# Performance work log

Measured on AMD Instinct MI355X. Metric: run time of the kernel, lower is better.

## Reference

```python
import jax, jax.numpy as jnp
import numpy as np

C = 256
CQK = C // 8  # query/key channels = int(in_dim // 8)

def _conv1x1(x, W, b):
    # x: [B,C,H,W], W: [O,C], b: [O] -> [B,O,H,W]
    return jnp.einsum('bchw,oc->bohw', x, W) + b[None, :, None, None]

def setup_inputs() -> dict:
    key = jax.random.key(0)
    ks = jax.random.split(key, 9)
    B, H, W = 4, 64, 64
    s = lambda fan_in: 1.0 / np.sqrt(fan_in)
    x = jax.random.normal(ks[0], (B, C, H, W), dtype=jnp.float32)
    Wq = jax.random.uniform(ks[1], (CQK, C), jnp.float32, -s(C), s(C))
    bq = jax.random.uniform(ks[2], (CQK,), jnp.float32, -s(C), s(C))
    Wk = jax.random.uniform(ks[3], (CQK, C), jnp.float32, -s(C), s(C))
    bk = jax.random.uniform(ks[4], (CQK,), jnp.float32, -s(C), s(C))
    Wv = jax.random.uniform(ks[5], (C, C), jnp.float32, -s(C), s(C))
    bv = jax.random.uniform(ks[6], (C,), jnp.float32, -s(C), s(C))
    Wo = jax.random.uniform(ks[7], (C, 2 * C), jnp.float32, -s(2 * C), s(2 * C))
    bo = jax.random.uniform(ks[8], (C,), jnp.float32, -s(2 * C), s(2 * C))
    return {"x": x, "Wq": Wq, "bq": bq, "Wk": Wk, "bk": bk,
            "Wv": Wv, "bv": bv, "Wo": Wo, "bo": bo}

def reference(x, Wq, bq, Wk, bk, Wv, bv, Wo, bo):
    B, Cc, H, W = x.shape
    N = H * W
    q = _conv1x1(x, Wq, bq).reshape(B, CQK, N)   # [B,Cqk,N]
    k = _conv1x1(x, Wk, bk).reshape(B, CQK, N)   # [B,Cqk,N]
    v = _conv1x1(x, Wv, bv).reshape(B, Cc, N)    # [B,C,N]
    # energy[b,m,n] = sum_c q[b,c,m] * k[b,c,n]
    energy = jnp.einsum('bcm,bcn->bmn', q, k)    # [B,N,N]
    attn = jax.nn.softmax(energy, axis=-1)
    # out[b,c,m] = sum_n v[b,c,n] * attn[b,m,n]
    out = jnp.einsum('bcn,bmn->bcm', v, attn).reshape(B, Cc, H, W)
    out = jnp.concatenate([out, x], axis=1)      # [B,2C,H,W]
    return _conv1x1(out, Wo, bo)                 # [B,C,H,W]
```

## Files before the change

kernel.cpp:

```cpp
#include <hip/hip_runtime.h>
#include <stdint.h>

typedef __attribute__((ext_vector_type(8))) __bf16 bf16x8;
typedef __attribute__((ext_vector_type(4))) float f32x4;
typedef __attribute__((ext_vector_type(16))) float f32x16;

#define MFMA16(a, b, c) __builtin_amdgcn_mfma_f32_16x16x32_bf16((a), (b), (c), 0, 0, 0)
#define MFMA32(a, b, c) __builtin_amdgcn_mfma_f32_32x32x16_bf16((a), (b), (c), 0, 0, 0)

__device__ __forceinline__ uint16_t f2b(float f) {
    union { float f; uint32_t u; } v; v.f = f;
    uint32_t u = v.u;
    return (uint16_t)((u + 0x7FFFu + ((u >> 16) & 1u)) >> 16);
}

__device__ __forceinline__ bf16x8 ldb8(const uint16_t* p) {
    return *(const bf16x8*)p;
}

__device__ __forceinline__ float exp2_fast(float x) {
#if __has_builtin(__builtin_amdgcn_exp2f)
    return __builtin_amdgcn_exp2f(x);
#else
    return __expf(x * 0.6931471805599453f);
#endif
}

__global__ void pack_kernel(const float* __restrict__ Wq, const float* __restrict__ Wk,
                            const float* __restrict__ Wv, const float* __restrict__ bq,
                            const float* __restrict__ bk, const float* __restrict__ bv,
                            const float* __restrict__ Wo,
                            uint16_t* __restrict__ Wall, uint16_t* __restrict__ Wobf,
                            float* __restrict__ ball) {
    const float LOG2E = 1.4426950408889634f;
    int i = blockIdx.x * blockDim.x + threadIdx.x;
    int stride = gridDim.x * blockDim.x;
    for (int idx = i; idx < 320 * 256; idx += stride) {
        int r = idx >> 8, c = idx & 255;
        float v = (r < 32) ? Wq[r * 256 + c] * LOG2E
                 : (r < 64) ? Wk[(r - 32) * 256 + c]
                            : Wv[(r - 64) * 256 + c];
        Wall[idx] = f2b(v);
    }
    for (int idx = i; idx < 256 * 512; idx += stride) Wobf[idx] = f2b(Wo[idx]);
    for (int idx = i; idx < 320; idx += stride)
        ball[idx] = (idx < 32) ? bq[idx] * LOG2E
                  : (idx < 64) ? bk[idx - 32] : bv[idx - 64];
}

__global__ __launch_bounds__(256) void qkv_kernel(
    const float* __restrict__ x, const uint16_t* __restrict__ Wall,
    const float* __restrict__ ball, uint16_t* __restrict__ qtg,
    uint16_t* __restrict__ ktg, uint16_t* __restrict__ vg) {
    __shared__ uint16_t xt[64][264];

    const int b = blockIdx.x >> 6;
    const int n0 = (blockIdx.x & 63) * 64;
    const int t = threadIdx.x;
    const float* xb = x + (size_t)b * 256 * 4096;

    {
        const int nPart = t & 15, cIdx = t >> 4;
#pragma unroll
        for (int rep = 0; rep < 16; rep++) {
            int c = rep * 16 + cIdx;
            float4 f = *(const float4*)(xb + (size_t)c * 4096 + n0 + nPart * 4);
            xt[nPart * 4 + 0][c] = f2b(f.x);
            xt[nPart * 4 + 1][c] = f2b(f.y);
            xt[nPart * 4 + 2][c] = f2b(f.z);
            xt[nPart * 4 + 3][c] = f2b(f.w);
        }
    }
    __syncthreads();

    const int w = t >> 6, lane = t & 63, l15 = lane & 15, g = lane >> 4;

    f32x4 accqk[4] = {};
#pragma unroll
    for (int ks = 0; ks < 8; ks++) {
        bf16x8 af = ldb8(&xt[w * 16 + l15][ks * 32 + g * 8]);
#pragma unroll
        for (int ot = 0; ot < 4; ot++) {
            bf16x8 bfr = ldb8(Wall + (ot * 16 + l15) * 256 + ks * 32 + g * 8);
            accqk[ot] = MFMA16(af, bfr, accqk[ot]);
        }
    }
#pragma unroll
    for (int ot = 0; ot < 4; ot++) {
        int o = ot * 16 + l15;
        float bias = ball[o];
#pragma unroll
        for (int r = 0; r < 4; r++) {
            int n = n0 + w * 16 + g * 4 + r;
            float v = accqk[ot][r] + bias;
            if (ot < 2) {
                qtg[((size_t)b * 4096 + n) * 32 + o] = f2b(v);
            } else {
                int c = o - 32;
                size_t idx = ((((size_t)b * 128 + (n >> 5)) * 2 + (c >> 4)) * 32
                              + (n & 31)) * 16 + (c & 15);
                ktg[idx] = f2b(v);
            }
        }
    }

    f32x4 accv[4][4] = {};
#pragma unroll
    for (int ks = 0; ks < 8; ks++) {
        bf16x8 av[4], bv4[4];
#pragma unroll
        for (int mt = 0; mt < 4; mt++)
            av[mt] = ldb8(Wall + (64 + (w * 4 + mt) * 16 + l15) * 256 + ks * 32 + g * 8);
#pragma unroll
        for (int nt = 0; nt < 4; nt++)
            bv4[nt] = ldb8(&xt[nt * 16 + l15][ks * 32 + g * 8]);
#pragma unroll
        for (int mt = 0; mt < 4; mt++)
#pragma unroll
            for (int nt = 0; nt < 4; nt++)
                accv[mt][nt] = MFMA16(av[mt], bv4[nt], accv[mt][nt]);
    }
#pragma unroll
    for (int mt = 0; mt < 4; mt++) {
#pragma unroll
        for (int r = 0; r < 4; r++) {
            int o = (w * 4 + mt) * 16 + g * 4 + r;
            float bias = ball[64 + o];
#pragma unroll
            for (int nt = 0; nt < 4; nt++) {
                int n = n0 + nt * 16 + l15;
                size_t idx = (((size_t)b * 512 + (n >> 3)) * 256 + o) * 8 + (n & 7);
                vg[idx] = f2b(accv[mt][nt][r] + bias);
            }
        }
    }
}

__global__ __launch_bounds__(256, 2) void attn_kernel(
    const uint16_t* __restrict__ qtg, const uint16_t* __restrict__ ktg,
    const uint16_t* __restrict__ vg, uint16_t* __restrict__ og) {
    __shared__ uint16_t pts[2][2][32][36];
    __shared__ float lsp[4][16];

    const int bid = blockIdx.x;
    const int swz = (bid & 7) * 64 + (bid >> 3);
    const int b = swz >> 7;
    const int m0 = (swz & 127) * 32;
    const int t = threadIdx.x, w = t >> 6, lane = t & 63;
    const int l15 = lane & 15, g = lane >> 4;
    const int l31 = lane & 31, hi = lane >> 5;
    const int mh = w >> 1, nhf = w & 1;

    const uint16_t* qb = qtg + (size_t)b * 4096 * 32;
    const uint16_t* kb = ktg + (size_t)b * 131072;
    const uint16_t* vb = vg  + (size_t)b * 1048576;

    const bf16x8 qf = ldb8(qb + (size_t)(m0 + mh * 16 + l15) * 32 + g * 8);
    const uint16_t* kbase = kb + (g >> 1) * 512 + (nhf * 16 + l15) * 16 + (g & 1) * 8;

    const int m_loc = mh * 16 + l15;
    const int wq = nhf * 4 + g;
    const int pwo = m_loc * 72 + wq * 8;

    int prd[2][2];
#pragma unroll
    for (int ks = 0; ks < 2; ks++) {
        prd[ks][0] = l31 * 72 + (ks * 4 + hi * 2) * 8;
        prd[ks][1] = l31 * 72 + (ks * 4 + hi * 2 + 1) * 8;
    }

    const uint16_t* vbase = vb + (size_t)hi * 2048 + (w * 64 + l31) * 8;

    f32x16 acc[2] = {};
    float lpart = 0.f;

    auto loadK = [&](int ch) -> bf16x8 { return ldb8(kbase + ch * 1024); };
    auto loadV = [&](int ch, bf16x8 (*vf)[2]) {
#pragma unroll
        for (int ct = 0; ct < 2; ct++)
#pragma unroll
            for (int ks = 0; ks < 2; ks++)
                vf[ct][ks] = ldb8(vbase + ch * 8192 + ks * 4096 + ct * 256);
    };

    auto sphase = [&](const bf16x8 kf, char* tilebase) {
        f32x4 z = {};
        f32x4 s = MFMA16(kf, qf, z);
        float e0 = exp2_fast(s[0]), e1 = exp2_fast(s[1]);
        float e2 = exp2_fast(s[2]), e3 = exp2_fast(s[3]);
        lpart += (e0 + e1) + (e2 + e3);
        union { uint2 d; __bf16 h[4]; } u;
        u.h[0] = (__bf16)e0; u.h[1] = (__bf16)e1;
        u.h[2] = (__bf16)e2; u.h[3] = (__bf16)e3;
        *(uint2*)(tilebase + pwo) = u.d;
    };
    auto pv = [&](const char* tilebase, const bf16x8 (*vf)[2]) {
        bf16x8 pa[2];
#pragma unroll
        for (int ks = 0; ks < 2; ks++) {
            union { bf16x8 v; uint2 dd[2]; } up;
            up.dd[0] = *(const uint2*)(tilebase + prd[ks][0]);
            up.dd[1] = *(const uint2*)(tilebase + prd[ks][1]);
            pa[ks] = up.v;
        }
        __builtin_amdgcn_s_setprio(1);
#pragma unroll
        for (int ks = 0; ks < 2; ks++)
#pragma unroll
            for (int ct = 0; ct < 2; ct++)
                acc[ct] = MFMA32(pa[ks], vf[ct][ks], acc[ct]);
        __builtin_amdgcn_s_setprio(0);
    };

    auto pbar = [&]() {
        asm volatile("s_waitcnt lgkmcnt(0)" ::: "memory");
        __builtin_amdgcn_s_barrier();
        __builtin_amdgcn_sched_barrier(0);
    };

    char* const buf0 = (char*)pts;
    char* const buf1 = (char*)pts + 4608;

    bf16x8 kpA[2], kpB[2];
    bf16x8 vpA0[2][2], vpA1[2][2], vpB0[2][2], vpB1[2][2];
    kpA[0] = loadK(0); kpA[1] = loadK(1); loadV(0, vpA0); loadV(1, vpA1);
    kpB[0] = loadK(2); kpB[1] = loadK(3); loadV(2, vpB0); loadV(3, vpB1);

    for (int j = 0; j < 64; j += 2) {
        sphase(kpA[0], buf0);
        sphase(kpA[1], buf0 + 2304);
        if (j + 2 < 64) { kpA[0] = loadK(2 * j + 4); kpA[1] = loadK(2 * j + 5); }
        pbar();
        pv(buf0, vpA0);
        pv(buf0 + 2304, vpA1);
        if (j + 2 < 64) { loadV(2 * j + 4, vpA0); loadV(2 * j + 5, vpA1); }
        sphase(kpB[0], buf1);
        sphase(kpB[1], buf1 + 2304);
        if (j + 3 < 64) { kpB[0] = loadK(2 * j + 6); kpB[1] = loadK(2 * j + 7); }
        pbar();
        pv(buf1, vpB0);
        pv(buf1 + 2304, vpB1);
        if (j + 3 < 64) { loadV(2 * j + 6, vpB0); loadV(2 * j + 7, vpB1); }
    }

    lpart += __shfl_xor(lpart, 16);
    lpart += __shfl_xor(lpart, 32);
    if (lane < 16) lsp[w][lane] = lpart;
    __syncthreads();

#pragma unroll
    for (int r = 0; r < 16; r++) {
        const int m = (r & 3) + 8 * (r >> 2) + 4 * hi;
        const float l = lsp[2 * (m >> 4)][m & 15] + lsp[2 * (m >> 4) + 1][m & 15];
        const float rinv = 1.0f / l;
        const size_t rowo = ((size_t)b * 4096 + m0 + m) * 256 + w * 64 + l31;
        og[rowo] = f2b(acc[0][r] * rinv);
        og[rowo + 32] = f2b(acc[1][r] * rinv);
    }
}

__global__ __launch_bounds__(256) void out_kernel(
    const float* __restrict__ x, const uint16_t* __restrict__ og,
    const uint16_t* __restrict__ Wobf, const float* __restrict__ bo,
    float* __restrict__ y) {
    __shared__ uint16_t xt[64][264];

    const int b = blockIdx.x >> 6;
    const int m0 = (blockIdx.x & 63) * 64;
    const int t = threadIdx.x;
    const float* xb = x + (size_t)b * 256 * 4096;

    {
        const int nPart = t & 15, cIdx = t >> 4;
#pragma unroll
        for (int rep = 0; rep < 16; rep++) {
            int c = rep * 16 + cIdx;
            float4 f = *(const float4*)(xb + (size_t)c * 4096 + m0 + nPart * 4);
            xt[nPart * 4 + 0][c] = f2b(f.x);
            xt[nPart * 4 + 1][c] = f2b(f.y);
            xt[nPart * 4 + 2][c] = f2b(f.z);
            xt[nPart * 4 + 3][c] = f2b(f.w);
        }
    }
    __syncthreads();

    const int w = t >> 6, lane = t & 63, l15 = lane & 15, g = lane >> 4;
    const uint16_t* ob = og + ((size_t)b * 4096 + m0) * 256;

    f32x4 acc[4][4] = {};
#pragma unroll
    for (int ks = 0; ks < 8; ks++) {
        bf16x8 af[4], bfr[4];
#pragma unroll
        for (int mt = 0; mt < 4; mt++)
            af[mt] = ldb8(Wobf + ((w * 4 + mt) * 16 + l15) * 512 + ks * 32 + g * 8);
#pragma unroll
        for (int nt = 0; nt < 4; nt++)
            bfr[nt] = ldb8(ob + (size_t)(nt * 16 + l15) * 256 + ks * 32 + g * 8);
#pragma unroll
        for (int mt = 0; mt < 4; mt++)
#pragma unroll
            for (int nt = 0; nt < 4; nt++)
                acc[mt][nt] = MFMA16(af[mt], bfr[nt], acc[mt][nt]);
    }
#pragma unroll
    for (int ks = 0; ks < 8; ks++) {
        bf16x8 af[4], bfr[4];
#pragma unroll
        for (int mt = 0; mt < 4; mt++)
            af[mt] = ldb8(Wobf + ((w * 4 + mt) * 16 + l15) * 512 + 256 + ks * 32 + g * 8);
#pragma unroll
        for (int nt = 0; nt < 4; nt++)
            bfr[nt] = ldb8(&xt[nt * 16 + l15][ks * 32 + g * 8]);
#pragma unroll
        for (int mt = 0; mt < 4; mt++)
#pragma unroll
            for (int nt = 0; nt < 4; nt++)
                acc[mt][nt] = MFMA16(af[mt], bfr[nt], acc[mt][nt]);
    }

#pragma unroll
    for (int mt = 0; mt < 4; mt++)
#pragma unroll
        for (int r = 0; r < 4; r++) {
            int o = (w * 4 + mt) * 16 + g * 4 + r;
            float bias = bo[o];
#pragma unroll
            for (int nt = 0; nt < 4; nt++) {
                int m = m0 + nt * 16 + l15;
                y[((size_t)b * 256 + o) * 4096 + m] = acc[mt][nt][r] + bias;
            }
        }
}

extern "C" void kernel_launch(void* const* d_in, const int* in_sizes, int n_in,
                              void* d_out, int out_size, void* d_ws, size_t ws_size,
                              hipStream_t stream) {
    const float* x  = (const float*)d_in[0];
    const float* Wq = (const float*)d_in[1];
    const float* bq = (const float*)d_in[2];
    const float* Wk = (const float*)d_in[3];
    const float* bk = (const float*)d_in[4];
    const float* Wv = (const float*)d_in[5];
    const float* bv = (const float*)d_in[6];
    const float* Wo = (const float*)d_in[7];
    const float* bo = (const float*)d_in[8];
    float* y = (float*)d_out;

    char* ws = (char*)d_ws;
    uint16_t* Wall = (uint16_t*)(ws + 0);
    uint16_t* Wobf = (uint16_t*)(ws + 163840);
    float*    ball = (float*)(ws + 425984);
    uint16_t* qtg  = (uint16_t*)(ws + 427520);
    uint16_t* ktg  = (uint16_t*)(ws + 1476096);
    uint16_t* vgw  = (uint16_t*)(ws + 2524672);
    uint16_t* ogw  = (uint16_t*)(ws + 10913280);

    pack_kernel<<<256, 256, 0, stream>>>(Wq, Wk, Wv, bq, bk, bv, Wo, Wall, Wobf, ball);
    qkv_kernel<<<256, 256, 0, stream>>>(x, Wall, ball, qtg, ktg, vgw);
    attn_kernel<<<512, 256, 0, stream>>>(qtg, ktg, vgw, ogw);
    out_kernel<<<256, 256, 0, stream>>>(x, ogw, Wobf, bo, y);
}
```

Before: 103.1 us.

## Enlarge attention tile to 64 query rows with 8 waves and LDS-staged K

```diff
diff --git a/kernel.cpp b/kernel.cpp
--- a/kernel.cpp
+++ b/kernel.cpp
@@ -136,54 +136,54 @@
     }
 }
 
-__global__ __launch_bounds__(256, 2) void attn_kernel(
+__global__ __launch_bounds__(512, 2) void attn_kernel(
     const uint16_t* __restrict__ qtg, const uint16_t* __restrict__ ktg,
     const uint16_t* __restrict__ vg, uint16_t* __restrict__ og) {
-    __shared__ uint16_t pts[2][2][32][36];
-    __shared__ float lsp[4][16];
+    __shared__ uint16_t pts[2][2][64][36];
+    __shared__ uint2 klds[2][512];
+    __shared__ float lsp[8][16];
 
     const int bid = blockIdx.x;
-    const int swz = (bid & 7) * 64 + (bid >> 3);
-    const int b = swz >> 7;
-    const int m0 = (swz & 127) * 32;
+    const int swz = (bid & 7) * 32 + (bid >> 3);
+    const int b = swz >> 6;
+    const int m0 = (swz & 63) * 64;
     const int t = threadIdx.x, w = t >> 6, lane = t & 63;
     const int l15 = lane & 15, g = lane >> 4;
     const int l31 = lane & 31, hi = lane >> 5;
-    const int mh = w >> 1, nhf = w & 1;
+    const int smh = w >> 1, snf = w & 1;
 
     const uint16_t* qb = qtg + (size_t)b * 4096 * 32;
     const uint16_t* kb = ktg + (size_t)b * 131072;
     const uint16_t* vb = vg  + (size_t)b * 1048576;
 
-    const bf16x8 qf = ldb8(qb + (size_t)(m0 + mh * 16 + l15) * 32 + g * 8);
-    const uint16_t* kbase = kb + (g >> 1) * 512 + (nhf * 16 + l15) * 16 + (g & 1) * 8;
-
-    const int m_loc = mh * 16 + l15;
-    const int wq = nhf * 4 + g;
+    const bf16x8 qf = ldb8(qb + (size_t)(m0 + smh * 16 + l15) * 32 + g * 8);
+    const int kfoff = ((g >> 1) * 512 + (snf * 16 + l15) * 16 + (g & 1) * 8) * 2;
+
+    const int m_loc = smh * 16 + l15;
+    const int wq = snf * 4 + g;
     const int pwo = m_loc * 72 + wq * 8;
 
-    int prd[2][2];
-#pragma unroll
-    for (int ks = 0; ks < 2; ks++) {
-        prd[ks][0] = l31 * 72 + (ks * 4 + hi * 2) * 8;
-        prd[ks][1] = l31 * 72 + (ks * 4 + hi * 2 + 1) * 8;
-    }
-
-    const uint16_t* vbase = vb + (size_t)hi * 2048 + (w * 64 + l31) * 8;
+    const uint16_t* vbase = vb + (size_t)hi * 2048 + (w * 32 + l31) * 8;
 
     f32x16 acc[2] = {};
     float lpart = 0.f;
-
-    auto loadK = [&](int ch) -> bf16x8 { return ldb8(kbase + ch * 1024); };
-    auto loadV = [&](int ch, bf16x8 (*vf)[2]) {
-#pragma unroll
-        for (int ct = 0; ct < 2; ct++)
+    uint2 kreg;
+
+    auto kload = [&](int q) -> uint2 {
+        return *(const uint2*)(kb + (size_t)q * 2048 + t * 4);
+    };
+    auto loadVpair = [&](int q, bf16x8 (*vp)[2]) {
+#pragma unroll
+        for (int cc = 0; cc < 2; cc++)
 #pragma unroll
             for (int ks = 0; ks < 2; ks++)
-                vf[ct][ks] = ldb8(vbase + ch * 8192 + ks * 4096 + ct * 256);
-    };
-
-    auto sphase = [&](const bf16x8 kf, char* tilebase) {
+                vp[cc][ks] = ldb8(vbase + (size_t)(2 * q + cc) * 8192 + ks * 4096);
+    };
+
+    auto sphase = [&](int pj, int cc) {
+        const uint16_t* ksrc =
+            (const uint16_t*)((const char*)klds + pj * 4096 + cc * 2048 + kfoff);
+        bf16x8 kf = ldb8(ksrc);
         f32x4 z = {};
         f32x4 s = MFMA16(kf, qf, z);
         float e0 = exp2_fast(s[0]), e1 = exp2_fast(s[1]);
@@ -192,23 +192,27 @@
         union { uint2 d; __bf16 h[4]; } u;
         u.h[0] = (__bf16)e0; u.h[1] = (__bf16)e1;
         u.h[2] = (__bf16)e2; u.h[3] = (__bf16)e3;
-        *(uint2*)(tilebase + pwo) = u.d;
-    };
-    auto pv = [&](const char* tilebase, const bf16x8 (*vf)[2]) {
-        bf16x8 pa[2];
-#pragma unroll
-        for (int ks = 0; ks < 2; ks++) {
-            union { bf16x8 v; uint2 dd[2]; } up;
-            up.dd[0] = *(const uint2*)(tilebase + prd[ks][0]);
-            up.dd[1] = *(const uint2*)(tilebase + prd[ks][1]);
-            pa[ks] = up.v;
-        }
+        *(uint2*)((char*)pts + pj * 9216 + cc * 4608 + pwo) = u.d;
+    };
+    auto pv = [&](int pj, int cc, const bf16x8* vf) {
+        const char* ptile = (const char*)pts + pj * 9216 + cc * 4608;
+        bf16x8 pa[2][2];
+#pragma unroll
+        for (int mh = 0; mh < 2; mh++)
+#pragma unroll
+            for (int ks = 0; ks < 2; ks++) {
+                union { bf16x8 v; uint2 dd[2]; } up;
+                const int base = (mh * 32 + l31) * 72 + (ks * 4 + hi * 2) * 8;
+                up.dd[0] = *(const uint2*)(ptile + base);
+                up.dd[1] = *(const uint2*)(ptile + base + 8);
+                pa[mh][ks] = up.v;
+            }
         __builtin_amdgcn_s_setprio(1);
 #pragma unroll
         for (int ks = 0; ks < 2; ks++)
 #pragma unroll
-            for (int ct = 0; ct < 2; ct++)
-                acc[ct] = MFMA32(pa[ks], vf[ct][ks], acc[ct]);
+            for (int mh = 0; mh < 2; mh++)
+                acc[mh] = MFMA32(pa[mh][ks], vf[ks], acc[mh]);
         __builtin_amdgcn_s_setprio(0);
     };
 
@@ -218,29 +222,28 @@
         __builtin_amdgcn_sched_barrier(0);
     };
 
-    char* const buf0 = (char*)pts;
-    char* const buf1 = (char*)pts + 4608;
-
-    bf16x8 kpA[2], kpB[2];
-    bf16x8 vpA0[2][2], vpA1[2][2], vpB0[2][2], vpB1[2][2];
-    kpA[0] = loadK(0); kpA[1] = loadK(1); loadV(0, vpA0); loadV(1, vpA1);
-    kpB[0] = loadK(2); kpB[1] = loadK(3); loadV(2, vpB0); loadV(3, vpB1);
+    auto phase = [&](int q, int pj, bf16x8 (*vp)[2]) {
+        if (q + 1 < 64) klds[pj ^ 1][t] = kreg;
+        sphase(pj, 0);
+        sphase(pj, 1);
+        if (q + 2 < 64) kreg = kload(q + 2);
+        pbar();
+        pv(pj, 0, vp[0]);
+        pv(pj, 1, vp[1]);
+        if (q + 2 < 64) loadVpair(q + 2, vp);
+    };
+
+    bf16x8 vpA[2][2], vpB[2][2];
+    uint2 kr0 = kload(0);
+    loadVpair(0, vpA);
+    loadVpair(1, vpB);
+    klds[0][t] = kr0;
+    kreg = kload(1);
+    pbar();
 
     for (int j = 0; j < 64; j += 2) {
-        sphase(kpA[0], buf0);
-        sphase(kpA[1], buf0 + 2304);
-        if (j + 2 < 64) { kpA[0] = loadK(2 * j + 4); kpA[1] = loadK(2 * j + 5); }
-        pbar();
-        pv(buf0, vpA0);
-        pv(buf0 + 2304, vpA1);
-        if (j + 2 < 64) { loadV(2 * j + 4, vpA0); loadV(2 * j + 5, vpA1); }
-        sphase(kpB[0], buf1);
-        sphase(kpB[1], buf1 + 2304);
-        if (j + 3 < 64) { kpB[0] = loadK(2 * j + 6); kpB[1] = loadK(2 * j + 7); }
-        pbar();
-        pv(buf1, vpB0);
-        pv(buf1 + 2304, vpB1);
-        if (j + 3 < 64) { loadV(2 * j + 6, vpB0); loadV(2 * j + 7, vpB1); }
+        phase(j, 0, vpA);
+        phase(j + 1, 1, vpB);
     }
 
     lpart += __shfl_xor(lpart, 16);
@@ -249,14 +252,16 @@
     __syncthreads();
 
 #pragma unroll
-    for (int r = 0; r < 16; r++) {
-        const int m = (r & 3) + 8 * (r >> 2) + 4 * hi;
-        const float l = lsp[2 * (m >> 4)][m & 15] + lsp[2 * (m >> 4) + 1][m & 15];
-        const float rinv = 1.0f / l;
-        const size_t rowo = ((size_t)b * 4096 + m0 + m) * 256 + w * 64 + l31;
-        og[rowo] = f2b(acc[0][r] * rinv);
-        og[rowo + 32] = f2b(acc[1][r] * rinv);
-    }
+    for (int mh = 0; mh < 2; mh++)
+#pragma unroll
+        for (int r = 0; r < 16; r++) {
+            const int rowm = (r & 3) + 8 * (r >> 2) + 4 * hi;
+            const int mrow = mh * 32 + rowm;
+            const float l = lsp[(mrow >> 4) * 2][mrow & 15]
+                          + lsp[(mrow >> 4) * 2 + 1][mrow & 15];
+            const size_t idx = ((size_t)b * 4096 + m0 + mrow) * 256 + w * 32 + l31;
+            og[idx] = f2b(acc[mh][r] / l);
+        }
 }
 
 __global__ __launch_bounds__(256) void out_kernel(
@@ -358,6 +363,6 @@
 
     pack_kernel<<<256, 256, 0, stream>>>(Wq, Wk, Wv, bq, bk, bv, Wo, Wall, Wobf, ball);
     qkv_kernel<<<256, 256, 0, stream>>>(x, Wall, ball, qtg, ktg, vgw);
-    attn_kernel<<<512, 256, 0, stream>>>(qtg, ktg, vgw, ogw);
+    attn_kernel<<<256, 512, 0, stream>>>(qtg, ktg, vgw, ogw);
     out_kernel<<<256, 256, 0, stream>>>(x, ogw, Wobf, bo, y);
 }
```

Result: slower. 115.1 us (+11.6%).
